# Optimization experiments

Hardware: AMD Instinct MI355X
Metric: run time of the kernel (lower is better)

The kernel has to match this reference:

```python
import jax, jax.numpy as jnp
import numpy as np

B = 512   # batch (== window_size, required by the original detrend loop)
W = 512   # window_size
E = 512   # emb_dim
EPS = 1e-5


def setup_inputs() -> dict:
    key = jax.random.key(0)
    k = jax.random.split(key, 5)
    x = jax.random.normal(k[0], (B, W, E), dtype=jnp.float32)
    # per-channel Linear(window_size, 1): stacked as [E, W] weights, [E] bias
    W1 = jax.random.normal(k[1], (E, W), dtype=jnp.float32) / np.sqrt(W)
    b1 = jax.random.normal(k[2], (E,), dtype=jnp.float32) * 0.01
    gamma = jnp.ones((E,), dtype=jnp.float32)   # BatchNorm1d(1) weight per channel
    beta = jnp.zeros((E,), dtype=jnp.float32)   # BatchNorm1d(1) bias per channel
    W2 = jax.random.normal(k[3], (E, 1), dtype=jnp.float32) / np.sqrt(E)
    b2 = jnp.zeros((1,), dtype=jnp.float32)
    return {"x": x, "W1": W1, "b1": b1, "gamma": gamma, "beta": beta, "W2": W2, "b2": b2}


def reference(x, W1, b1, gamma, beta, W2, b2):
    # seq_last is detached in the original (no grad through this path)
    seq_last = jax.lax.stop_gradient(x[:, -1, :])          # [B, E]
    xd = x - seq_last[:, None, :]                          # detrend all timesteps
    # E independent Linear(W -> 1), vectorized as one contraction
    lin = jnp.einsum('bwe,ew->be', xd, W1) + b1            # [B, E]
    # BatchNorm1d(1) per channel, training mode: biased var over batch
    mean = jnp.mean(lin, axis=0)                           # [E]
    var = jnp.mean((lin - mean) ** 2, axis=0)              # [E], biased
    bn = (lin - mean) * jax.lax.rsqrt(var + EPS) * gamma + beta
    out = bn + seq_last                                    # [B, E]
    return out @ W2 + b2                                   # [B, 1]
```

## Files before the change

kernel.cpp:

```cpp
#include <hip/hip_runtime.h>
#include <math.h>

#define Bn 512
#define Wn 512
#define En 512
#define WSPLIT 4
#define WCH (Wn / WSPLIT)
#define EPSF 1e-5f

#define O_W1T    0
#define O_SUMW1  (O_W1T + En * Wn)
#define O_PART   (O_SUMW1 + En)
#define O_LIN    (O_PART + WSPLIT * Bn * En)
#define O_PSUM   (O_LIN + Bn * En)
#define O_PSUMSQ (O_PSUM + 8 * En)
#define O_SCALE  (O_PSUMSQ + 8 * En)
#define O_SHIFT  (O_SCALE + En)

__global__ void k_transpose(const float* __restrict__ w1, float* __restrict__ w1t) {
    __shared__ float tile[32][33];
    int bx = blockIdx.x, by = blockIdx.y;
    int tx = threadIdx.x, ty = threadIdx.y;
#pragma unroll
    for (int j = 0; j < 32; j += 8)
        tile[ty + j][tx] = w1[(size_t)(by * 32 + ty + j) * Wn + bx * 32 + tx];
    __syncthreads();
#pragma unroll
    for (int j = 0; j < 32; j += 8)
        w1t[(size_t)(bx * 32 + ty + j) * En + by * 32 + tx] = tile[tx][ty + j];
}

__global__ void k_sumw1(const float* __restrict__ w1, float* __restrict__ sumw1) {
    int e = blockIdx.x;
    int l = threadIdx.x;
    const float* row = w1 + (size_t)e * Wn;
    float s = 0.f;
#pragma unroll
    for (int j = 0; j < Wn; j += 64) s += row[j + l];
#pragma unroll
    for (int off = 32; off; off >>= 1) s += __shfl_down(s, off);
    if (l == 0) sumw1[e] = s;
}

__global__ __launch_bounds__(128) void k_lin_partial(const float* __restrict__ x,
                                                     const float* __restrict__ w1t,
                                                     float* __restrict__ part) {
    int b = blockIdx.x, wc = blockIdx.y;
    int e4 = threadIdx.x;
    const float4* xp = (const float4*)x + ((size_t)b * Wn + (size_t)wc * WCH) * (En / 4) + e4;
    const float4* wp = (const float4*)w1t + (size_t)(wc * WCH) * (En / 4) + e4;
    float ax = 0.f, ay = 0.f, az = 0.f, aw = 0.f;
#pragma unroll 4
    for (int w = 0; w < WCH; ++w) {
        float4 xv = xp[(size_t)w * (En / 4)];
        float4 wv = wp[(size_t)w * (En / 4)];
        ax += xv.x * wv.x;
        ay += xv.y * wv.y;
        az += xv.z * wv.z;
        aw += xv.w * wv.w;
    }
    float4 r;
    r.x = ax; r.y = ay; r.z = az; r.w = aw;
    ((float4*)part)[((size_t)wc * Bn + b) * (En / 4) + e4] = r;
}

__global__ __launch_bounds__(128) void k_lin_reduce(const float* __restrict__ part,
                                                    const float* __restrict__ x,
                                                    const float* __restrict__ sumw1,
                                                    const float* __restrict__ b1,
                                                    float* __restrict__ lin) {
    int b = blockIdx.x;
    int e4 = threadIdx.x;
    const float4* p = (const float4*)part;
    float sx = 0.f, sy = 0.f, sz = 0.f, sw = 0.f;
#pragma unroll
    for (int wc = 0; wc < WSPLIT; ++wc) {
        float4 v = p[((size_t)wc * Bn + b) * (En / 4) + e4];
        sx += v.x; sy += v.y; sz += v.z; sw += v.w;
    }
    float4 xl = ((const float4*)x)[((size_t)b * Wn + (Wn - 1)) * (En / 4) + e4];
    float4 s1 = ((const float4*)sumw1)[e4];
    float4 bb = ((const float4*)b1)[e4];
    float4 r;
    r.x = sx - xl.x * s1.x + bb.x;
    r.y = sy - xl.y * s1.y + bb.y;
    r.z = sz - xl.z * s1.z + bb.z;
    r.w = sw - xl.w * s1.w + bb.w;
    ((float4*)lin)[(size_t)b * (En / 4) + e4] = r;
}

__global__ void k_stats_partial(const float* __restrict__ lin,
                                float* __restrict__ psum, float* __restrict__ psumsq) {
    int blk = blockIdx.x;
    int e = threadIdx.x;
    float s = 0.f, q = 0.f;
    int b0 = blk * 64;
    for (int b = b0; b < b0 + 64; ++b) {
        float v = lin[(size_t)b * En + e];
        s += v;
        q += v * v;
    }
    psum[blk * En + e] = s;
    psumsq[blk * En + e] = q;
}

__global__ void k_stats_final(const float* __restrict__ psum, const float* __restrict__ psumsq,
                              const float* __restrict__ gamma, const float* __restrict__ beta,
                              float* __restrict__ scale, float* __restrict__ shift) {
    int e = threadIdx.x;
    float s = 0.f, q = 0.f;
#pragma unroll
    for (int c = 0; c < 8; ++c) {
        s += psum[c * En + e];
        q += psumsq[c * En + e];
    }
    float mean = s * (1.f / Bn);
    float var = q * (1.f / Bn) - mean * mean;
    float sc = gamma[e] * rsqrtf(var + EPSF);
    scale[e] = sc;
    shift[e] = beta[e] - mean * sc;
}

__global__ __launch_bounds__(128) void k_out(const float* __restrict__ lin,
                                             const float* __restrict__ x,
                                             const float* __restrict__ scale,
                                             const float* __restrict__ shift,
                                             const float* __restrict__ w2,
                                             const float* __restrict__ b2,
                                             float* __restrict__ out) {
    int b = blockIdx.x;
    int t = threadIdx.x;
    float4 l  = ((const float4*)lin)[(size_t)b * (En / 4) + t];
    float4 xl = ((const float4*)x)[((size_t)b * Wn + (Wn - 1)) * (En / 4) + t];
    float4 sc = ((const float4*)scale)[t];
    float4 sh = ((const float4*)shift)[t];
    float4 wv = ((const float4*)w2)[t];
    float v = (l.x * sc.x + sh.x + xl.x) * wv.x
            + (l.y * sc.y + sh.y + xl.y) * wv.y
            + (l.z * sc.z + sh.z + xl.z) * wv.z
            + (l.w * sc.w + sh.w + xl.w) * wv.w;
#pragma unroll
    for (int off = 32; off; off >>= 1) v += __shfl_down(v, off);
    __shared__ float red[2];
    int wid = t >> 6, lane = t & 63;
    if (lane == 0) red[wid] = v;
    __syncthreads();
    if (t == 0) out[b] = red[0] + red[1] + b2[0];
}

extern "C" void kernel_launch(void* const* d_in, const int* in_sizes, int n_in,
                              void* d_out, int out_size, void* d_ws, size_t ws_size,
                              hipStream_t stream) {
    const float* x     = (const float*)d_in[0];
    const float* w1    = (const float*)d_in[1];
    const float* b1    = (const float*)d_in[2];
    const float* gamma = (const float*)d_in[3];
    const float* beta  = (const float*)d_in[4];
    const float* w2    = (const float*)d_in[5];
    const float* b2    = (const float*)d_in[6];
    float* out = (float*)d_out;
    float* ws  = (float*)d_ws;

    float* w1t    = ws + O_W1T;
    float* sumw1  = ws + O_SUMW1;
    float* part   = ws + O_PART;
    float* lin    = ws + O_LIN;
    float* psum   = ws + O_PSUM;
    float* psumsq = ws + O_PSUMSQ;
    float* scale  = ws + O_SCALE;
    float* shift  = ws + O_SHIFT;

    k_transpose<<<dim3(Wn / 32, En / 32), dim3(32, 8), 0, stream>>>(w1, w1t);
    k_sumw1<<<En, 64, 0, stream>>>(w1, sumw1);
    k_lin_partial<<<dim3(Bn, WSPLIT), 128, 0, stream>>>(x, w1t, part);
    k_lin_reduce<<<Bn, 128, 0, stream>>>(part, x, sumw1, b1, lin);
    k_stats_partial<<<8, 512, 0, stream>>>(lin, psum, psumsq);
    k_stats_final<<<1, 512, 0, stream>>>(psum, psumsq, gamma, beta, scale, shift);
    k_out<<<Bn, 128, 0, stream>>>(lin, x, scale, shift, w2, b2, out);
}
```

Before: 120.6 us.

## Fuse W-split partials, sum(W1) and reduce into one block-wide kernel

Replaces the separate sum-of-W1, partial-contraction and reduce kernels with a single 512-thread kernel per batch row. Its four W-chunks are reduced through shared memory, and it accumulates the row sums of W1 on the fly. The BN finalize step moves into the output kernel, so each block recomputes scale and shift. Together this removes three launches and the 4MB partial buffer round-trip. It also adds nontemporal loads for x, at the cost of redundant W1-sum and stats work in every block.

New measurement: 108.1 us. 10.4% less time.

```diff
diff --git a/kernel.cpp b/kernel.cpp
--- a/kernel.cpp
+++ b/kernel.cpp
@@ -4,18 +4,14 @@
 #define Bn 512
 #define Wn 512
 #define En 512
-#define WSPLIT 4
-#define WCH (Wn / WSPLIT)
 #define EPSF 1e-5f
 
+typedef float fx4 __attribute__((ext_vector_type(4)));
+
 #define O_W1T    0
-#define O_SUMW1  (O_W1T + En * Wn)
-#define O_PART   (O_SUMW1 + En)
-#define O_LIN    (O_PART + WSPLIT * Bn * En)
+#define O_LIN    (O_W1T + En * Wn)
 #define O_PSUM   (O_LIN + Bn * En)
 #define O_PSUMSQ (O_PSUM + 8 * En)
-#define O_SCALE  (O_PSUMSQ + 8 * En)
-#define O_SHIFT  (O_SCALE + En)
 
 __global__ void k_transpose(const float* __restrict__ w1, float* __restrict__ w1t) {
     __shared__ float tile[32][33];
@@ -30,63 +26,46 @@
         w1t[(size_t)(bx * 32 + ty + j) * En + by * 32 + tx] = tile[tx][ty + j];
 }
 
-__global__ void k_sumw1(const float* __restrict__ w1, float* __restrict__ sumw1) {
-    int e = blockIdx.x;
-    int l = threadIdx.x;
-    const float* row = w1 + (size_t)e * Wn;
-    float s = 0.f;
+__global__ __launch_bounds__(512) void k_main(const float* __restrict__ x,
+                                              const float* __restrict__ w1t,
+                                              const float* __restrict__ b1,
+                                              float* __restrict__ lin) {
+    int b = blockIdx.x;
+    int tid = threadIdx.x;
+    int wsub = tid >> 7;
+    int e4 = tid & 127;
+
+    const fx4* xp = (const fx4*)x + ((size_t)b * Wn + (size_t)wsub * 128) * (En / 4) + e4;
+    const fx4* wp = (const fx4*)w1t + (size_t)(wsub * 128) * (En / 4) + e4;
+
+    fx4 acc = {0.f, 0.f, 0.f, 0.f};
+    fx4 wsum = {0.f, 0.f, 0.f, 0.f};
+#pragma unroll 8
+    for (int w = 0; w < 128; ++w) {
+        fx4 xv = __builtin_nontemporal_load(&xp[(size_t)w * (En / 4)]);
+        fx4 wv = wp[(size_t)w * (En / 4)];
+        acc += xv * wv;
+        wsum += wv;
+    }
+
+    __shared__ fx4 lacc[4][128];
+    __shared__ fx4 lws[4][128];
+    lacc[wsub][e4] = acc;
+    lws[wsub][e4] = wsum;
+    __syncthreads();
+
+    if (wsub == 0) {
+        fx4 t = lacc[0][e4], u = lws[0][e4];
 #pragma unroll
-    for (int j = 0; j < Wn; j += 64) s += row[j + l];
-#pragma unroll
-    for (int off = 32; off; off >>= 1) s += __shfl_down(s, off);
-    if (l == 0) sumw1[e] = s;
-}
-
-__global__ __launch_bounds__(128) void k_lin_partial(const float* __restrict__ x,
-                                                     const float* __restrict__ w1t,
-                                                     float* __restrict__ part) {
-    int b = blockIdx.x, wc = blockIdx.y;
-    int e4 = threadIdx.x;
-    const float4* xp = (const float4*)x + ((size_t)b * Wn + (size_t)wc * WCH) * (En / 4) + e4;
-    const float4* wp = (const float4*)w1t + (size_t)(wc * WCH) * (En / 4) + e4;
-    float ax = 0.f, ay = 0.f, az = 0.f, aw = 0.f;
-#pragma unroll 4
-    for (int w = 0; w < WCH; ++w) {
-        float4 xv = xp[(size_t)w * (En / 4)];
-        float4 wv = wp[(size_t)w * (En / 4)];
-        ax += xv.x * wv.x;
-        ay += xv.y * wv.y;
-        az += xv.z * wv.z;
-        aw += xv.w * wv.w;
+        for (int k = 1; k < 4; ++k) {
+            t += lacc[k][e4];
+            u += lws[k][e4];
+        }
+        fx4 xl = ((const fx4*)x)[((size_t)b * Wn + (Wn - 1)) * (En / 4) + e4];
+        fx4 bb = ((const fx4*)b1)[e4];
+        fx4 r = t - xl * u + bb;
+        ((fx4*)lin)[(size_t)b * (En / 4) + e4] = r;
     }
-    float4 r;
-    r.x = ax; r.y = ay; r.z = az; r.w = aw;
-    ((float4*)part)[((size_t)wc * Bn + b) * (En / 4) + e4] = r;
-}
-
-__global__ __launch_bounds__(128) void k_lin_reduce(const float* __restrict__ part,
-                                                    const float* __restrict__ x,
-                                                    const float* __restrict__ sumw1,
-                                                    const float* __restrict__ b1,
-                                                    float* __restrict__ lin) {
-    int b = blockIdx.x;
-    int e4 = threadIdx.x;
-    const float4* p = (const float4*)part;
-    float sx = 0.f, sy = 0.f, sz = 0.f, sw = 0.f;
-#pragma unroll
-    for (int wc = 0; wc < WSPLIT; ++wc) {
-        float4 v = p[((size_t)wc * Bn + b) * (En / 4) + e4];
-        sx += v.x; sy += v.y; sz += v.z; sw += v.w;
-    }
-    float4 xl = ((const float4*)x)[((size_t)b * Wn + (Wn - 1)) * (En / 4) + e4];
-    float4 s1 = ((const float4*)sumw1)[e4];
-    float4 bb = ((const float4*)b1)[e4];
-    float4 r;
-    r.x = sx - xl.x * s1.x + bb.x;
-    r.y = sy - xl.y * s1.y + bb.y;
-    r.z = sz - xl.z * s1.z + bb.z;
-    r.w = sw - xl.w * s1.w + bb.w;
-    ((float4*)lin)[(size_t)b * (En / 4) + e4] = r;
 }
 
 __global__ void k_stats_partial(const float* __restrict__ lin,
@@ -95,6 +74,7 @@
     int e = threadIdx.x;
     float s = 0.f, q = 0.f;
     int b0 = blk * 64;
+#pragma unroll 4
     for (int b = b0; b < b0 + 64; ++b) {
         float v = lin[(size_t)b * En + e];
         s += v;
@@ -104,41 +84,38 @@
     psumsq[blk * En + e] = q;
 }
 
-__global__ void k_stats_final(const float* __restrict__ psum, const float* __restrict__ psumsq,
-                              const float* __restrict__ gamma, const float* __restrict__ beta,
-                              float* __restrict__ scale, float* __restrict__ shift) {
-    int e = threadIdx.x;
-    float s = 0.f, q = 0.f;
-#pragma unroll
-    for (int c = 0; c < 8; ++c) {
-        s += psum[c * En + e];
-        q += psumsq[c * En + e];
-    }
-    float mean = s * (1.f / Bn);
-    float var = q * (1.f / Bn) - mean * mean;
-    float sc = gamma[e] * rsqrtf(var + EPSF);
-    scale[e] = sc;
-    shift[e] = beta[e] - mean * sc;
-}
-
 __global__ __launch_bounds__(128) void k_out(const float* __restrict__ lin,
                                              const float* __restrict__ x,
-                                             const float* __restrict__ scale,
-                                             const float* __restrict__ shift,
+                                             const float* __restrict__ psum,
+                                             const float* __restrict__ psumsq,
+                                             const float* __restrict__ gamma,
+                                             const float* __restrict__ beta,
                                              const float* __restrict__ w2,
                                              const float* __restrict__ b2,
                                              float* __restrict__ out) {
     int b = blockIdx.x;
     int t = threadIdx.x;
-    float4 l  = ((const float4*)lin)[(size_t)b * (En / 4) + t];
-    float4 xl = ((const float4*)x)[((size_t)b * Wn + (Wn - 1)) * (En / 4) + t];
-    float4 sc = ((const float4*)scale)[t];
-    float4 sh = ((const float4*)shift)[t];
-    float4 wv = ((const float4*)w2)[t];
-    float v = (l.x * sc.x + sh.x + xl.x) * wv.x
-            + (l.y * sc.y + sh.y + xl.y) * wv.y
-            + (l.z * sc.z + sh.z + xl.z) * wv.z
-            + (l.w * sc.w + sh.w + xl.w) * wv.w;
+
+    fx4 s4 = {0.f, 0.f, 0.f, 0.f}, q4 = {0.f, 0.f, 0.f, 0.f};
+#pragma unroll
+    for (int c = 0; c < 8; ++c) {
+        s4 += ((const fx4*)psum)[c * (En / 4) + t];
+        q4 += ((const fx4*)psumsq)[c * (En / 4) + t];
+    }
+    fx4 g = ((const fx4*)gamma)[t];
+    fx4 be = ((const fx4*)beta)[t];
+    fx4 mean = s4 * (1.f / Bn);
+    fx4 var = q4 * (1.f / Bn) - mean * mean;
+    fx4 sc, sh;
+    sc.x = g.x * rsqrtf(var.x + EPSF); sc.y = g.y * rsqrtf(var.y + EPSF);
+    sc.z = g.z * rsqrtf(var.z + EPSF); sc.w = g.w * rsqrtf(var.w + EPSF);
+    sh = be - mean * sc;
+
+    fx4 l  = ((const fx4*)lin)[(size_t)b * (En / 4) + t];
+    fx4 xl = ((const fx4*)x)[((size_t)b * Wn + (Wn - 1)) * (En / 4) + t];
+    fx4 wv = ((const fx4*)w2)[t];
+    fx4 term = (l * sc + sh + xl) * wv;
+    float v = term.x + term.y + term.z + term.w;
 #pragma unroll
     for (int off = 32; off; off >>= 1) v += __shfl_down(v, off);
     __shared__ float red[2];
@@ -162,19 +139,12 @@
     float* ws  = (float*)d_ws;
 
     float* w1t    = ws + O_W1T;
-    float* sumw1  = ws + O_SUMW1;
-    float* part   = ws + O_PART;
     float* lin    = ws + O_LIN;
     float* psum   = ws + O_PSUM;
     float* psumsq = ws + O_PSUMSQ;
-    float* scale  = ws + O_SCALE;
-    float* shift  = ws + O_SHIFT;
 
     k_transpose<<<dim3(Wn / 32, En / 32), dim3(32, 8), 0, stream>>>(w1, w1t);
-    k_sumw1<<<En, 64, 0, stream>>>(w1, sumw1);
-    k_lin_partial<<<dim3(Bn, WSPLIT), 128, 0, stream>>>(x, w1t, part);
-    k_lin_reduce<<<Bn, 128, 0, stream>>>(part, x, sumw1, b1, lin);
+    k_main<<<Bn, 512, 0, stream>>>(x, w1t, b1, lin);
     k_stats_partial<<<8, 512, 0, stream>>>(lin, psum, psumsq);
-    k_stats_final<<<1, 512, 0, stream>>>(psum, psumsq, gamma, beta, scale, shift);
-    k_out<<<Bn, 128, 0, stream>>>(lin, x, scale, shift, w2, b2, out);
+    k_out<<<Bn, 128, 0, stream>>>(lin, x, psum, psumsq, gamma, beta, w2, b2, out);
 }
```
